# Kernel optimization log

Measured on AMD Instinct MI355X. Metric: run time of the kernel, lower is better.

Reference implementation:

```python
import jax, jax.numpy as jnp
import numpy as np

B, T, I, H, C, S = 512, 128, 512, 512, 97, 26  # batch, enc_len, input, hidden, classes, num_steps


def setup_inputs() -> dict:
    key = jax.random.key(0)
    ks = jax.random.split(key, 12)
    s = 0.05
    d = {}
    d["batch_H"] = jax.random.normal(ks[0], (B, T, I), dtype=jnp.float32)
    d["text"] = jax.random.randint(ks[1], (B, S), 0, C)
    # attention cell params
    d["W_feat"] = jax.random.normal(ks[2], (H, I), dtype=jnp.float32) * s   # feature_projection (no bias)
    d["W_hid"] = jax.random.normal(ks[3], (H, H), dtype=jnp.float32) * s    # hidden_projection
    d["b_hid"] = jnp.zeros((H,), dtype=jnp.float32)
    d["w_score"] = jax.random.normal(ks[4], (H,), dtype=jnp.float32) * s    # attention_score (Linear(H,1), no bias)
    # LSTMCell params, PyTorch gate order [i, f, g, o]
    d["W_ih"] = jax.random.normal(ks[5], (4 * H, I + C), dtype=jnp.float32) * s
    d["W_hh"] = jax.random.normal(ks[6], (4 * H, H), dtype=jnp.float32) * s
    d["b_ih"] = jnp.zeros((4 * H,), dtype=jnp.float32)
    d["b_hh"] = jnp.zeros((4 * H,), dtype=jnp.float32)
    # generator
    d["W_gen"] = jax.random.normal(ks[7], (C, H), dtype=jnp.float32) * s
    d["b_gen"] = jnp.zeros((C,), dtype=jnp.float32)
    return d


def reference(batch_H, text, W_feat, W_hid, b_hid, w_score, W_ih, W_hh, b_ih, b_hh, W_gen, b_gen):
    Bb, Tt, _ = batch_H.shape
    Hh = W_hid.shape[0]
    Cc = W_gen.shape[0]
    # step-invariant: project encoder features once  [B, T, H]
    feat = jnp.einsum('bti,hi->bth', batch_H, W_feat)
    onehots = jax.nn.one_hot(text, Cc, dtype=batch_H.dtype)  # [B, S, C]

    def step(carry, oh):
        h, c = carry
        hp = h @ W_hid.T + b_hid                                     # [B, H]
        e = jnp.einsum('bth,h->bt', jnp.tanh(feat + hp[:, None, :]), w_score)
        alpha = jax.nn.softmax(e, axis=1)                            # [B, T]
        ctx = jnp.einsum('bt,bti->bi', alpha, batch_H)               # [B, I]
        x = jnp.concatenate([ctx, oh], axis=1)                       # [B, I+C]
        gates = x @ W_ih.T + b_ih + h @ W_hh.T + b_hh                # [B, 4H]
        i_g, f_g, g_g, o_g = jnp.split(gates, 4, axis=1)
        c2 = jax.nn.sigmoid(f_g) * c + jax.nn.sigmoid(i_g) * jnp.tanh(g_g)
        h2 = jax.nn.sigmoid(o_g) * jnp.tanh(c2)
        return (h2, c2), h2

    init = (jnp.zeros((Bb, Hh), dtype=batch_H.dtype), jnp.zeros((Bb, Hh), dtype=batch_H.dtype))
    _, hs = jax.lax.scan(step, init, jnp.swapaxes(onehots, 0, 1))    # hs: [S, B, H]
    out_h = jnp.swapaxes(hs, 0, 1)                                   # [B, S, H]
    probs = out_h @ W_gen.T + b_gen                                  # [B, S, C]
    return probs
```

## Files before the change

### kernel.cpp

```cpp
#include <hip/hip_runtime.h>
#include <hip/hip_bf16.h>
#include <stdint.h>
#include <stddef.h>

typedef __bf16 bf16;
typedef __bf16 v8bf __attribute__((ext_vector_type(8)));
typedef float  v4f  __attribute__((ext_vector_type(4)));

#define B_ 512
#define T_ 128
#define I_ 512
#define H_ 512
#define C_ 97
#define S_ 26

__device__ __forceinline__ void async_copy16(void* lds, const void* g) {
  __builtin_amdgcn_global_load_lds((__attribute__((address_space(1))) void*)g,
                                   (__attribute__((address_space(3))) void*)lds,
                                   16, 0, 0);
}

__device__ __forceinline__ float fast_tanh(float x) {
  float e = __expf(2.0f * x);
  return fmaf(-2.0f, __builtin_amdgcn_rcpf(e + 1.0f), 1.0f);
}
__device__ __forceinline__ float fast_sigmoid(float x) {
  float t = __expf(-x);
  return __builtin_amdgcn_rcpf(1.0f + t);
}

__device__ __forceinline__ void zero_acc(v4f acc[4][4]) {
  v4f z = {0.f, 0.f, 0.f, 0.f};
#pragma unroll
  for (int i = 0; i < 4; ++i)
#pragma unroll
    for (int j = 0; j < 4; ++j) acc[i][j] = z;
}

#define WAITBAR(N)                                             \
  do {                                                         \
    asm volatile("s_waitcnt vmcnt(" #N ")" ::: "memory");      \
    __builtin_amdgcn_s_barrier();                              \
    __builtin_amdgcn_sched_barrier(0);                         \
  } while (0)

template <int KTOT>
__device__ __forceinline__ void mm_qb32(const bf16* aRow0, const bf16* aRow1,
                                        const bf16* bRow0, const bf16* bRow1,
                                        bf16* As, bf16* Bs, int tid,
                                        v4f acc[4][4]) {
  constexpr int NT = KTOT / 32;
  const int wave = tid >> 6, lane = tid & 63;
  const int wr = (wave >> 1) * 64, wc = (wave & 1) * 64;
  const int fr = lane & 15, fq = lane >> 4;
  const int s0 = tid * 8;
  const int aB = (wr + fr) * 32 + fq * 8;
  const int bB = (wc + fr) * 32 + fq * 8;
#define STG32(bi, kk)                                   \
  do {                                                  \
    const int o = (bi) * 4096 + s0;                     \
    async_copy16(As + o, aRow0 + (kk));                 \
    async_copy16(As + o + 2048, aRow1 + (kk));          \
    async_copy16(Bs + o, bRow0 + (kk));                 \
    async_copy16(Bs + o + 2048, bRow1 + (kk));          \
  } while (0)
  STG32(0, 0);
  STG32(1, 32);
  for (int t = 0; t < NT; ++t) {
    if (t + 2 < NT) {
      STG32((t + 2) & 3, (t + 2) * 32);
      WAITBAR(8);
    } else if (t + 1 < NT) {
      WAITBAR(4);
    } else {
      WAITBAR(0);
    }
    const int cb = (t & 3) * 4096;
    v8bf av[4], bv[4];
#pragma unroll
    for (int i = 0; i < 4; ++i) av[i] = *(const v8bf*)(As + cb + aB + i * 512);
#pragma unroll
    for (int j = 0; j < 4; ++j) bv[j] = *(const v8bf*)(Bs + cb + bB + j * 512);
    __builtin_amdgcn_s_setprio(1);
#pragma unroll
    for (int i = 0; i < 4; ++i) {
#pragma unroll
      for (int j = 0; j < 4; ++j) {
        acc[i][j] = __builtin_amdgcn_mfma_f32_16x16x32_bf16(av[i], bv[j], acc[i][j], 0, 0, 0);
      }
    }
    __builtin_amdgcn_s_setprio(0);
  }
#undef STG32
}

template <int KTOT>
__device__ __forceinline__ void mm_reg_f32a(const float* aR0, const float* aR1,
                                            const bf16* bRow0, const bf16* bRow1,
                                            bf16* As, bf16* Bs, int tid,
                                            v4f acc[4][4]) {
  const int wave = tid >> 6, lane = tid & 63;
  const int wr = (wave >> 1) * 64, wc = (wave & 1) * 64;
  const int fr = lane & 15, fq = lane >> 4;
  bf16* a_s0 = As + tid * 8;
  bf16* a_s1 = As + (tid + 256) * 8;
  bf16* b_s0 = Bs + tid * 8;
  bf16* b_s1 = Bs + (tid + 256) * 8;
  const bf16* aF[4];
  const bf16* bF[4];
#pragma unroll
  for (int i = 0; i < 4; ++i) {
    aF[i] = As + (wr + i * 16 + fr) * 32 + fq * 8;
    bF[i] = Bs + (wc + i * 16 + fr) * 32 + fq * 8;
  }
  for (int kk = 0; kk < KTOT; kk += 32) {
    v8bf va0, va1;
    const float* p0 = aR0 + kk;
    const float* p1 = aR1 + kk;
    v4f f00 = ((const v4f*)p0)[0], f01 = ((const v4f*)p0)[1];
    v4f f10 = ((const v4f*)p1)[0], f11 = ((const v4f*)p1)[1];
#pragma unroll
    for (int j = 0; j < 4; ++j) {
      va0[j] = (bf16)f00[j]; va0[j + 4] = (bf16)f01[j];
      va1[j] = (bf16)f10[j]; va1[j + 4] = (bf16)f11[j];
    }
    v8bf vb0 = *(const v8bf*)(bRow0 + kk);
    v8bf vb1 = *(const v8bf*)(bRow1 + kk);
    __syncthreads();
    *(v8bf*)a_s0 = va0;
    *(v8bf*)a_s1 = va1;
    *(v8bf*)b_s0 = vb0;
    *(v8bf*)b_s1 = vb1;
    __syncthreads();
    v8bf av[4], bv[4];
#pragma unroll
    for (int i = 0; i < 4; ++i) av[i] = *(const v8bf*)aF[i];
#pragma unroll
    for (int j = 0; j < 4; ++j) bv[j] = *(const v8bf*)bF[j];
#pragma unroll
    for (int i = 0; i < 4; ++i) {
#pragma unroll
      for (int j = 0; j < 4; ++j) {
        acc[i][j] = __builtin_amdgcn_mfma_f32_16x16x32_bf16(av[i], bv[j], acc[i][j], 0, 0, 0);
      }
    }
  }
  __syncthreads();
}

__global__ void k_prep_all(const float* __restrict__ batch_H, bf16* __restrict__ bH16, int nbh,
                           const float* __restrict__ W_feat, bf16* __restrict__ Wf16,
                           const float* __restrict__ W_hid, bf16* __restrict__ Whid16,
                           const float* __restrict__ Wih, const float* __restrict__ Whh,
                           bf16* __restrict__ Wcat,
                           const float* __restrict__ Wg, bf16* __restrict__ Wgen16,
                           float* __restrict__ OHT) {
  int b = blockIdx.x;
  const int t = threadIdx.x;
  if (b < nbh) {
    int i = (b * 256 + t) * 4;
    v4f f = *(const v4f*)(batch_H + i);
#pragma unroll
    for (int j = 0; j < 4; ++j) bH16[i + j] = (bf16)f[j];
    return;
  }
  b -= nbh;
  if (b < 256) {
    int i = (b * 256 + t) * 4;
    v4f f = *(const v4f*)(W_feat + i);
#pragma unroll
    for (int j = 0; j < 4; ++j) Wf16[i + j] = (bf16)f[j];
  } else if (b < 512) {
    int i = ((b - 256) * 256 + t) * 4;
    v4f f = *(const v4f*)(W_hid + i);
#pragma unroll
    for (int j = 0; j < 4; ++j) Whid16[i + j] = (bf16)f[j];
  } else if (b < 2560) {
    int n = b - 512;
#pragma unroll
    for (int j = 0; j < 4; ++j) {
      int k = t * 4 + j;
      float v = (k < 512) ? Wih[(size_t)n * 609 + k] : Whh[(size_t)n * 512 + (k - 512)];
      Wcat[(size_t)n * 1024 + k] = (bf16)v;
    }
  } else if (b < 2688) {
    int row = b - 2560;
#pragma unroll
    for (int j = 0; j < 2; ++j) {
      int k = t * 2 + j;
      float v = (row < C_) ? Wg[(size_t)row * 512 + k] : 0.0f;
      Wgen16[(size_t)row * 512 + k] = (bf16)v;
    }
  } else {
    int n = (b - 2688) * 256 + t;
    const float* src = Wih + (size_t)n * 609 + 512;
    for (int c = 0; c < C_; ++c) OHT[(size_t)c * 2048 + n] = src[c];
  }
}


__global__ __launch_bounds__(256, 2) void k_feat16(const bf16* __restrict__ A,
                                                   const bf16* __restrict__ Bw,
                                                   bf16* __restrict__ F) {
  __shared__ bf16 As[4 * 4096];
  __shared__ bf16 Bs[4 * 4096];
  const int tid = threadIdx.x;
  const int m0 = blockIdx.x * 128, n0 = blockIdx.y * 128;
  const int r0 = tid >> 2, k0 = (tid & 3) * 8;
  const bf16* aRow0 = A + (size_t)(m0 + r0) * 512 + k0;
  const bf16* aRow1 = A + (size_t)(m0 + r0 + 64) * 512 + k0;
  const bf16* bRow0 = Bw + (size_t)(n0 + r0) * 512 + k0;
  const bf16* bRow1 = Bw + (size_t)(n0 + r0 + 64) * 512 + k0;
  v4f acc[4][4];
  zero_acc(acc);
  mm_qb32<512>(aRow0, aRow1, bRow0, bRow1, As, Bs, tid, acc);
  const int wave = tid >> 6, lane = tid & 63;
  const int wr = (wave >> 1) * 64, wc = (wave & 1) * 64;
  const int fr = lane & 15, fq = lane >> 4;
#pragma unroll
  for (int i = 0; i < 4; ++i) {
#pragma unroll
    for (int j = 0; j < 4; ++j) {
      int col = n0 + wc + j * 16 + fr;
#pragma unroll
      for (int r = 0; r < 4; ++r) {
        int row = m0 + wr + i * 16 + fq * 4 + r;
        F[(size_t)row * 512 + col] = (bf16)acc[i][j][r];
      }
    }
  }
}

__global__ __launch_bounds__(256, 2) void k_feat32(const float* __restrict__ A,
                                                   const bf16* __restrict__ Bw,
                                                   bf16* __restrict__ F) {
  __shared__ bf16 As[128 * 32];
  __shared__ bf16 Bs[128 * 32];
  const int tid = threadIdx.x;
  const int m0 = blockIdx.x * 128, n0 = blockIdx.y * 128;
  const int r0 = tid >> 2, k0 = (tid & 3) * 8;
  const float* aRow0 = A + (size_t)(m0 + r0) * 512 + k0;
  const float* aRow1 = A + (size_t)(m0 + r0 + 64) * 512 + k0;
  const bf16* bRow0 = Bw + (size_t)(n0 + r0) * 512 + k0;
  const bf16* bRow1 = Bw + (size_t)(n0 + r0 + 64) * 512 + k0;
  v4f acc[4][4];
  zero_acc(acc);
  mm_reg_f32a<512>(aRow0, aRow1, bRow0, bRow1, As, Bs, tid, acc);
  const int wave = tid >> 6, lane = tid & 63;
  const int wr = (wave >> 1) * 64, wc = (wave & 1) * 64;
  const int fr = lane & 15, fq = lane >> 4;
#pragma unroll
  for (int i = 0; i < 4; ++i) {
#pragma unroll
    for (int j = 0; j < 4; ++j) {
      int col = n0 + wc + j * 16 + fr;
#pragma unroll
      for (int r = 0; r < 4; ++r) {
        int row = m0 + wr + i * 16 + fq * 4 + r;
        F[(size_t)row * 512 + col] = (bf16)acc[i][j][r];
      }
    }
  }
}

__global__ __launch_bounds__(256) void k_hp(const bf16* __restrict__ xb_cur,
                                            const bf16* __restrict__ Whid16,
                                            const float* __restrict__ b_hid,
                                            float* __restrict__ P) {
  __shared__ bf16 As[4 * 2048];
  __shared__ bf16 Bs[4 * 4096];
  const int tid = threadIdx.x, wave = tid >> 6, lane = tid & 63;
  const int flat = blockIdx.x;
  const int m0 = (flat >> 3) * 32;
  const int n0 = (flat & 7) * 64;
  const int fr = lane & 15, fq = lane >> 4;
  const int ra = tid >> 3, sa = (tid & 7) ^ (ra & 7);
  const bf16* aSrc = xb_cur + (size_t)(m0 + ra) * 1024 + 512 + sa * 8;
  const int rb0 = tid >> 3, rb1 = (tid >> 3) + 32;
  const bf16* bSrc0 = Whid16 + (size_t)(n0 + rb0) * 512 + (((tid & 7) ^ (rb0 & 7)) * 8);
  const bf16* bSrc1 = Whid16 + (size_t)(n0 + rb1) * 512 + (((tid & 7) ^ (rb1 & 7)) * 8);
  const int s0 = tid * 8;
  v4f acc[2];
  v4f z = {0.f, 0.f, 0.f, 0.f};
  acc[0] = z; acc[1] = z;
#define STGH(bi, kk)                                    \
  do {                                                  \
    async_copy16(As + (bi) * 2048 + s0, aSrc + (kk));   \
    async_copy16(Bs + (bi) * 4096 + s0, bSrc0 + (kk));  \
    async_copy16(Bs + (bi) * 4096 + 2048 + s0, bSrc1 + (kk)); \
  } while (0)
  STGH(0, 0);
  STGH(1, 64);
  constexpr int NT = 8;
  for (int t = 0; t < NT; ++t) {
    if (t + 2 < NT) {
      STGH((t + 2) & 3, (t + 2) * 64);
      WAITBAR(6);
    } else if (t + 1 < NT) {
      WAITBAR(3);
    } else {
      WAITBAR(0);
    }
    const int cb4 = (t & 3) * 2048;
    const int cb8 = (t & 3) * 4096;
#pragma unroll
    for (int ks = 0; ks < 2; ++ks) {
      const int sw = ((ks * 4 + fq) ^ (fr & 7)) * 8;
      v8bf bv = *(const v8bf*)(Bs + cb8 + (wave * 16 + fr) * 64 + sw);
      __builtin_amdgcn_s_setprio(1);
#pragma unroll
      for (int i = 0; i < 2; ++i) {
        v8bf av = *(const v8bf*)(As + cb4 + (i * 16 + fr) * 64 + sw);
        acc[i] = __builtin_amdgcn_mfma_f32_16x16x32_bf16(av, bv, acc[i], 0, 0, 0);
      }
      __builtin_amdgcn_s_setprio(0);
    }
  }
#undef STGH
  const int col = n0 + wave * 16 + fr;
  const float bh = b_hid[col];
#pragma unroll
  for (int i = 0; i < 2; ++i) {
#pragma unroll
    for (int r = 0; r < 4; ++r) {
      int row = m0 + i * 16 + fq * 4 + r;
      P[(size_t)row * 512 + col] = acc[i][r] + bh;
    }
  }
}

template <bool CTX16>
__global__ __launch_bounds__(512, 4) void k_attn(const bf16* __restrict__ F,
                                                 const float* __restrict__ P,
                                                 const float* __restrict__ w_score,
                                                 const void* __restrict__ bHv,
                                                 bf16* __restrict__ xb_cur) {
  const int b = blockIdx.x;
  const int tid = threadIdx.x, wave = tid >> 6, lane = tid & 63;
  __shared__ float e_s[T_];
  __shared__ float red[8][I_];
  const float CF = 2.8853900817779268f;
  float pl[8], Wv[8];
  {
    const float* p = P + (size_t)b * H_ + lane * 8;
#pragma unroll
    for (int j = 0; j < 8; ++j) pl[j] = CF * p[j];
    const float* w = w_score + lane * 8;
#pragma unroll
    for (int j = 0; j < 8; ++j) Wv[j] = w[j];
  }
  float sW = 0.f;
#pragma unroll
  for (int j = 0; j < 8; ++j) sW += Wv[j];
#pragma unroll
  for (int off = 32; off; off >>= 1) sW += __shfl_xor(sW, off, 64);
  const bf16* Fb = F + (size_t)b * T_ * H_ + lane * 8;
#pragma unroll
  for (int kb = 0; kb < 2; ++kb) {
    v8bf r[8];
#pragma unroll
    for (int u = 0; u < 8; ++u)
      r[u] = *(const v8bf*)(Fb + (size_t)(wave + kb * 64 + u * 8) * H_);
    float a[8];
#pragma unroll
    for (int u = 0; u < 8; ++u) {
      float s = 0.f;
#pragma unroll
      for (int j = 0; j < 8; ++j)
        s = fmaf(Wv[j], __builtin_amdgcn_rcpf(1.0f + exp2f(fmaf(CF, (float)r[u][j], pl[j]))), s);
      a[u] = s;
    }
#pragma unroll
    for (int off = 32; off; off >>= 1) {
#pragma unroll
      for (int u = 0; u < 8; ++u) a[u] += __shfl_xor(a[u], off, 64);
    }
    if (lane == 0) {
#pragma unroll
      for (int u = 0; u < 8; ++u) e_s[wave + kb * 64 + u * 8] = sW - 2.0f * a[u];
    }
  }
  __syncthreads();
  const int i0 = lane * 8;
  float c[8];
#pragma unroll
  for (int j = 0; j < 8; ++j) c[j] = 0.f;
  if (CTX16) {
    const bf16* hb = (const bf16*)bHv + (size_t)b * T_ * I_ + i0;
    v8bf p[8];
#pragma unroll
    for (int u = 0; u < 8; ++u)
      p[u] = *(const v8bf*)(hb + (size_t)(wave + u * 8) * I_);
    float x0, x1;
    {
      float e0 = e_s[lane], e1 = e_s[lane + 64];
      float m = fmaxf(e0, e1);
#pragma unroll
      for (int off = 32; off; off >>= 1) m = fmaxf(m, __shfl_xor(m, off, 64));
      x0 = __expf(e0 - m);
      x1 = __expf(e1 - m);
      float ssum = x0 + x1;
#pragma unroll
      for (int off = 32; off; off >>= 1) ssum += __shfl_xor(ssum, off, 64);
      float inv = __builtin_amdgcn_rcpf(ssum);
      x0 *= inv;
      x1 *= inv;
    }
    float aa[8];
#pragma unroll
    for (int u = 0; u < 8; ++u) aa[u] = __shfl(x0, wave + u * 8, 64);
    v8bf p2[8];
#pragma unroll
    for (int u = 0; u < 8; ++u)
      p2[u] = *(const v8bf*)(hb + (size_t)(64 + wave + u * 8) * I_);
#pragma unroll
    for (int u = 0; u < 8; ++u) {
#pragma unroll
      for (int j = 0; j < 8; ++j) c[j] = fmaf(aa[u], (float)p[u][j], c[j]);
    }
#pragma unroll
    for (int u = 0; u < 8; ++u) aa[u] = __shfl(x1, wave + u * 8, 64);
#pragma unroll
    for (int u = 0; u < 8; ++u) {
#pragma unroll
      for (int j = 0; j < 8; ++j) c[j] = fmaf(aa[u], (float)p2[u][j], c[j]);
    }
  } else {
    float x0, x1;
    {
      float e0 = e_s[lane], e1 = e_s[lane + 64];
      float m = fmaxf(e0, e1);
#pragma unroll
      for (int off = 32; off; off >>= 1) m = fmaxf(m, __shfl_xor(m, off, 64));
      x0 = __expf(e0 - m);
      x1 = __expf(e1 - m);
      float ssum = x0 + x1;
#pragma unroll
      for (int off = 32; off; off >>= 1) ssum += __shfl_xor(ssum, off, 64);
      float inv = __builtin_amdgcn_rcpf(ssum);
      x0 *= inv;
      x1 *= inv;
    }
    const float* hf = (const float*)bHv + (size_t)b * T_ * I_ + i0;
#pragma unroll
    for (int k = 0; k < 4; ++k) {
      const int t = wave + 32 * k;
      float xa = (k < 2) ? x0 : x1;
      float aa0 = __shfl(xa, t & 63, 64);
      float aa1 = __shfl(xa, (t + 8) & 63, 64);
      float aa2 = __shfl(xa, (t + 16) & 63, 64);
      float aa3 = __shfl(xa, (t + 24) & 63, 64);
      const float* p0 = hf + (size_t)t * I_;
      const float* p1 = hf + (size_t)(t + 8) * I_;
      const float* p2 = hf + (size_t)(t + 16) * I_;
      const float* p3 = hf + (size_t)(t + 24) * I_;
      v4f q00 = ((const v4f*)p0)[0], q01 = ((const v4f*)p0)[1];
      v4f q10 = ((const v4f*)p1)[0], q11 = ((const v4f*)p1)[1];
      v4f q20 = ((const v4f*)p2)[0], q21 = ((const v4f*)p2)[1];
      v4f q30 = ((const v4f*)p3)[0], q31 = ((const v4f*)p3)[1];
#pragma unroll
      for (int j = 0; j < 4; ++j) {
        c[j]     = fmaf(aa0, q00[j], c[j]);
        c[j + 4] = fmaf(aa0, q01[j], c[j + 4]);
        c[j]     = fmaf(aa1, q10[j], c[j]);
        c[j + 4] = fmaf(aa1, q11[j], c[j + 4]);
        c[j]     = fmaf(aa2, q20[j], c[j]);
        c[j + 4] = fmaf(aa2, q21[j], c[j + 4]);
        c[j]     = fmaf(aa3, q30[j], c[j]);
        c[j + 4] = fmaf(aa3, q31[j], c[j + 4]);
      }
    }
  }
#pragma unroll
  for (int j = 0; j < 8; ++j) red[wave][i0 + j] = c[j];
  __syncthreads();
  {
    int i = tid;
    float s = red[0][i] + red[1][i] + red[2][i] + red[3][i] +
              red[4][i] + red[5][i] + red[6][i] + red[7][i];
    xb_cur[(size_t)b * 1024 + i] = (bf16)s;
  }
}

__global__ __launch_bounds__(256) void k_gates(const bf16* __restrict__ xb_cur,
                                               const bf16* __restrict__ Wcat,
                                               const float* __restrict__ OHT,
                                               const float* __restrict__ b_ih,
                                               const float* __restrict__ b_hh,
                                               const int* __restrict__ text,
                                               float* __restrict__ c_state,
                                               bf16* __restrict__ out_h,
                                               bf16* __restrict__ xb_nxt, int s) {
  __shared__ union {
    struct { bf16 A[4 * 2048]; bf16 Bv[4 * 8192]; } st;
    float Cs[32 * 132];
  } sm;
  const int tid = threadIdx.x;
  const int flat = blockIdx.x;
  const int xcd = flat & 7;
  const int idx = flat >> 3;
  const int m0 = (idx >> 1) * 32;
  const int j0 = (xcd * 2 + (idx & 1)) * 32;
  const int wave = tid >> 6, lane = tid & 63;
  const int fr = lane & 15, fq = lane >> 4;
  const int s0 = tid * 8;
  const int ra = tid >> 3, sa = (tid & 7) ^ (ra & 7);
  const bf16* aSrc = xb_cur + (size_t)(m0 + ra) * 1024 + sa * 8;
  const bf16* bSrc[4];
#pragma unroll
  for (int cc = 0; cc < 4; ++cc) {
    const int rb = (tid >> 3) + cc * 32;
    const int nw = (rb >> 5) * 512 + j0 + (rb & 31);
    bSrc[cc] = Wcat + (size_t)nw * 1024 + (((tid & 7) ^ (rb & 7)) * 8);
  }
  v4f acc[2][2];
  {
    v4f z = {0.f, 0.f, 0.f, 0.f};
    acc[0][0] = z; acc[0][1] = z; acc[1][0] = z; acc[1][1] = z;
  }
#define STGG(bi, kk)                                                 \
  do {                                                               \
    async_copy16(sm.st.A + (bi) * 2048 + s0, aSrc + (kk));           \
    async_copy16(sm.st.Bv + (bi) * 8192 + s0, bSrc[0] + (kk));       \
    async_copy16(sm.st.Bv + (bi) * 8192 + 2048 + s0, bSrc[1] + (kk)); \
    async_copy16(sm.st.Bv + (bi) * 8192 + 4096 + s0, bSrc[2] + (kk)); \
    async_copy16(sm.st.Bv + (bi) * 8192 + 6144 + s0, bSrc[3] + (kk)); \
  } while (0)
  STGG(0, 0);
  STGG(1, 64);
  constexpr int NT = 16;
  for (int t = 0; t < NT; ++t) {
    if (t + 2 < NT) {
      STGG((t + 2) & 3, (t + 2) * 64);
      WAITBAR(10);
    } else if (t + 1 < NT) {
      WAITBAR(5);
    } else {
      WAITBAR(0);
    }
    const int ca = (t & 3) * 2048;
    const int cbv = (t & 3) * 8192;
#pragma unroll
    for (int ks = 0; ks < 2; ++ks) {
      const int sw = ((ks * 4 + fq) ^ (fr & 7)) * 8;
      v8bf av[2], bv[2];
#pragma unroll
      for (int i = 0; i < 2; ++i)
        av[i] = *(const v8bf*)(sm.st.A + ca + (i * 16 + fr) * 64 + sw);
#pragma unroll
      for (int jf = 0; jf < 2; ++jf)
        bv[jf] = *(const v8bf*)(sm.st.Bv + cbv + (wave * 32 + jf * 16 + fr) * 64 + sw);
      __builtin_amdgcn_s_setprio(1);
#pragma unroll
      for (int i = 0; i < 2; ++i)
#pragma unroll
        for (int jf = 0; jf < 2; ++jf)
          acc[i][jf] = __builtin_amdgcn_mfma_f32_16x16x32_bf16(av[i], bv[jf], acc[i][jf], 0, 0, 0);
      __builtin_amdgcn_s_setprio(0);
    }
  }
#undef STGG
  __syncthreads();
  int tcv[2][4];
#pragma unroll
  for (int i = 0; i < 2; ++i)
#pragma unroll
    for (int r = 0; r < 4; ++r)
      tcv[i][r] = text[(size_t)(m0 + i * 16 + fq * 4 + r) * S_ + s];
#pragma unroll
  for (int jf = 0; jf < 2; ++jf) {
    int cl = wave * 32 + jf * 16 + fr;
    int nw = (cl >> 5) * 512 + j0 + (cl & 31);
    float bias = b_ih[nw] + b_hh[nw];
    const float* oh = OHT + nw;
#pragma unroll
    for (int i = 0; i < 2; ++i) {
#pragma unroll
      for (int r = 0; r < 4; ++r) {
        int rl = i * 16 + fq * 4 + r;
        sm.Cs[rl * 132 + cl] = acc[i][jf][r] + bias + oh[(size_t)tcv[i][r] * 2048];
      }
    }
  }
  __syncthreads();
#pragma unroll
  for (int it = 0; it < 4; ++it) {
    int idx2 = tid + it * 256;
    int r = idx2 >> 5, q = idx2 & 31;
    float ig = sm.Cs[r * 132 + q];
    float fg = sm.Cs[r * 132 + 32 + q];
    float gg = sm.Cs[r * 132 + 64 + q];
    float og = sm.Cs[r * 132 + 96 + q];
    size_t cix = (size_t)(m0 + r) * 512 + j0 + q;
    float c2 = fast_sigmoid(fg) * c_state[cix] + fast_sigmoid(ig) * fast_tanh(gg);
    float h2 = fast_sigmoid(og) * fast_tanh(c2);
    c_state[cix] = c2;
    bf16 hb = (bf16)h2;
    xb_nxt[(size_t)(m0 + r) * 1024 + 512 + j0 + q] = hb;
    out_h[((size_t)(m0 + r) * S_ + s) * 512 + j0 + q] = hb;
  }
}

__global__ __launch_bounds__(256) void k_gen(const bf16* __restrict__ out_h,
                                             const bf16* __restrict__ Wgen16,
                                             const float* __restrict__ b_gen,
                                             float* __restrict__ out) {
  __shared__ bf16 As[4 * 4096];
  __shared__ bf16 Bs[4 * 4096];
  const int tid = threadIdx.x;
  const int m0 = blockIdx.x * 128;
  const int r0 = tid >> 2, k0 = (tid & 3) * 8;
  const bf16* aRow0 = out_h + (size_t)(m0 + r0) * 512 + k0;
  const bf16* aRow1 = out_h + (size_t)(m0 + r0 + 64) * 512 + k0;
  const bf16* bRow0 = Wgen16 + (size_t)r0 * 512 + k0;
  const bf16* bRow1 = Wgen16 + (size_t)(r0 + 64) * 512 + k0;
  v4f acc[4][4];
  zero_acc(acc);
  mm_qb32<512>(aRow0, aRow1, bRow0, bRow1, As, Bs, tid, acc);
  const int wave = tid >> 6, lane = tid & 63;
  const int wr = (wave >> 1) * 64, wc = (wave & 1) * 64;
  const int fr = lane & 15, fq = lane >> 4;
#pragma unroll
  for (int i = 0; i < 4; ++i) {
#pragma unroll
    for (int j = 0; j < 4; ++j) {
      int col = wc + j * 16 + fr;
      if (col < C_) {
        float bg = b_gen[col];
#pragma unroll
        for (int r = 0; r < 4; ++r) {
          int row = m0 + wr + i * 16 + fq * 4 + r;
          out[(size_t)row * C_ + col] = acc[i][j][r] + bg;
        }
      }
    }
  }
}

extern "C" void kernel_launch(void* const* d_in, const int* in_sizes, int n_in,
                              void* d_out, int out_size, void* d_ws, size_t ws_size,
                              hipStream_t stream) {
  (void)in_sizes; (void)n_in; (void)out_size;
  const float* batch_H = (const float*)d_in[0];
  const int*   text    = (const int*)d_in[1];
  const float* W_feat  = (const float*)d_in[2];
  const float* W_hid   = (const float*)d_in[3];
  const float* b_hid   = (const float*)d_in[4];
  const float* w_score = (const float*)d_in[5];
  const float* W_ih    = (const float*)d_in[6];
  const float* W_hh    = (const float*)d_in[7];
  const float* b_ih    = (const float*)d_in[8];
  const float* b_hh    = (const float*)d_in[9];
  const float* W_gen   = (const float*)d_in[10];
  const float* b_gen   = (const float*)d_in[11];
  float* out = (float*)d_out;

  char* ws = (char*)d_ws;
  bf16*  F       = (bf16*)(ws);
  bf16*  out_h   = (bf16*)(ws + 67108864);
  float* P       = (float*)(ws + 80740352);
  bf16*  xb0     = (bf16*)(ws + 81788928);
  bf16*  xb1     = (bf16*)(ws + 82837504);
  float* c_state = (float*)(ws + 83886080);
  bf16*  Wcat    = (bf16*)(ws + 84934656);
  bf16*  Wf16    = (bf16*)(ws + 89128960);
  bf16*  Whid16  = (bf16*)(ws + 89653248);
  bf16*  Wgen16  = (bf16*)(ws + 90177536);
  float* OHT     = (float*)(ws + 90308608);
  bf16*  bH16    = (bf16*)(ws + 91357184);
  const bool useBH16 = (ws_size >= (size_t)158466048);

  bf16* xb[2] = {xb0, xb1};

  hipMemsetAsync(xb0, 0, (size_t)512 * 1024 * 2, stream);
  hipMemsetAsync(c_state, 0, (size_t)512 * 512 * 4, stream);

  const int nbh = useBH16 ? 32768 : 0;
  k_prep_all<<<dim3(nbh + 2696), 256, 0, stream>>>(
      batch_H, bH16, nbh, W_feat, Wf16, W_hid, Whid16,
      W_ih, W_hh, Wcat, W_gen, Wgen16, OHT);

  if (useBH16) {
    k_feat16<<<dim3(512, 4), 256, 0, stream>>>(bH16, Wf16, F);
  } else {
    k_feat32<<<dim3(512, 4), 256, 0, stream>>>(batch_H, Wf16, F);
  }

  for (int s = 0; s < S_; ++s) {
    bf16* cur = xb[s & 1];
    bf16* nxt = xb[(s + 1) & 1];
    k_hp<<<dim3(128), 256, 0, stream>>>(cur, Whid16, b_hid, P);
    if (useBH16) {
      k_attn<true><<<dim3(512), 512, 0, stream>>>(F, P, w_score, bH16, cur);
    } else {
      k_attn<false><<<dim3(512), 512, 0, stream>>>(F, P, w_score, batch_H, cur);
    }
    k_gates<<<dim3(256), 256, 0, stream>>>(cur, Wcat, OHT, b_ih, b_hh, text,
                                           c_state, out_h, nxt, s);
  }
  k_gen<<<dim3(104, 1), 256, 0, stream>>>(out_h, Wgen16, b_gen, out);
}
```

Before: 1.441 ms.

## Split attention into parallel score kernel and context kernel; vectorize prep conversions

The fused per-batch attention kernel becomes two kernels. The first spreads the tanh-score computation over 2048 blocks (four per batch row) and writes scores to a scratch buffer, reusing the next-step xb buffer. The second does softmax and the context reduction. The prep kernel is reordered so the slow OHT transpose blocks launch first, and its bf16 conversions are vectorized to 8- and 4-element packed stores. This adds a kernel launch and a global round-trip of the scores each step, in exchange for more parallelism on the transcendental-heavy score phase.

Measured after the change: 1.478 ms. 2.5% more time.

```diff
diff --git a/kernel.cpp b/kernel.cpp
--- a/kernel.cpp
+++ b/kernel.cpp
@@ -35,6 +35,19 @@
   for (int i = 0; i < 4; ++i)
 #pragma unroll
     for (int j = 0; j < 4; ++j) acc[i][j] = z;
+}
+
+__device__ __forceinline__ void store_bf16x8(bf16* dst, v4f a, v4f b) {
+  union { bf16 h[8]; uint4 u; } pk;
+#pragma unroll
+  for (int j = 0; j < 4; ++j) { pk.h[j] = (bf16)a[j]; pk.h[4 + j] = (bf16)b[j]; }
+  *(uint4*)dst = pk.u;
+}
+__device__ __forceinline__ void store_bf16x4(bf16* dst, float a0, float a1,
+                                             float a2, float a3) {
+  union { bf16 h[4]; uint2 u; } pk;
+  pk.h[0] = (bf16)a0; pk.h[1] = (bf16)a1; pk.h[2] = (bf16)a2; pk.h[3] = (bf16)a3;
+  *(uint2*)dst = pk.u;
 }
 
 #define WAITBAR(N)                                             \
@@ -148,7 +161,7 @@
   __syncthreads();
 }
 
-__global__ void k_prep_all(const float* __restrict__ batch_H, bf16* __restrict__ bH16, int nbh,
+__global__ void k_prep_all(const float* __restrict__ batch_H, bf16* __restrict__ bH16, int nbhb,
                            const float* __restrict__ W_feat, bf16* __restrict__ Wf16,
                            const float* __restrict__ W_hid, bf16* __restrict__ Whid16,
                            const float* __restrict__ Wih, const float* __restrict__ Whh,
@@ -157,44 +170,61 @@
                            float* __restrict__ OHT) {
   int b = blockIdx.x;
   const int t = threadIdx.x;
-  if (b < nbh) {
-    int i = (b * 256 + t) * 4;
-    v4f f = *(const v4f*)(batch_H + i);
-#pragma unroll
-    for (int j = 0; j < 4; ++j) bH16[i + j] = (bf16)f[j];
+  if (b < 8) {
+    int n = b * 256 + t;
+    const float* src = Wih + (size_t)n * 609 + 512;
+#pragma unroll 8
+    for (int c = 0; c < C_; ++c) OHT[(size_t)c * 2048 + n] = src[c];
     return;
   }
-  b -= nbh;
-  if (b < 256) {
-    int i = (b * 256 + t) * 4;
-    v4f f = *(const v4f*)(W_feat + i);
-#pragma unroll
-    for (int j = 0; j < 4; ++j) Wf16[i + j] = (bf16)f[j];
-  } else if (b < 512) {
-    int i = ((b - 256) * 256 + t) * 4;
-    v4f f = *(const v4f*)(W_hid + i);
-#pragma unroll
-    for (int j = 0; j < 4; ++j) Whid16[i + j] = (bf16)f[j];
-  } else if (b < 2560) {
-    int n = b - 512;
-#pragma unroll
-    for (int j = 0; j < 4; ++j) {
-      int k = t * 4 + j;
-      float v = (k < 512) ? Wih[(size_t)n * 609 + k] : Whh[(size_t)n * 512 + (k - 512)];
-      Wcat[(size_t)n * 1024 + k] = (bf16)v;
-    }
-  } else if (b < 2688) {
-    int row = b - 2560;
-#pragma unroll
-    for (int j = 0; j < 2; ++j) {
-      int k = t * 2 + j;
-      float v = (row < C_) ? Wg[(size_t)row * 512 + k] : 0.0f;
-      Wgen16[(size_t)row * 512 + k] = (bf16)v;
-    }
-  } else {
-    int n = (b - 2688) * 256 + t;
-    const float* src = Wih + (size_t)n * 609 + 512;
-    for (int c = 0; c < C_; ++c) OHT[(size_t)c * 2048 + n] = src[c];
+  b -= 8;
+  if (b < 128) {
+    int row = b;
+    int k = t * 2;
+    float v0 = (row < C_) ? Wg[(size_t)row * 512 + k] : 0.0f;
+    float v1 = (row < C_) ? Wg[(size_t)row * 512 + k + 1] : 0.0f;
+    union { bf16 h[2]; uint u; } pk;
+    pk.h[0] = (bf16)v0; pk.h[1] = (bf16)v1;
+    *(uint*)(Wgen16 + (size_t)row * 512 + k) = pk.u;
+    return;
+  }
+  b -= 128;
+  if (b < 2048) {
+    int n = b;
+    int k = t * 4;
+    float v0, v1, v2, v3;
+    if (k < 512) {
+      const float* s = Wih + (size_t)n * 609 + k;
+      v0 = s[0]; v1 = s[1]; v2 = s[2]; v3 = s[3];
+    } else {
+      const float* s = Whh + (size_t)n * 512 + (k - 512);
+      v0 = s[0]; v1 = s[1]; v2 = s[2]; v3 = s[3];
+    }
+    store_bf16x4(Wcat + (size_t)n * 1024 + k, v0, v1, v2, v3);
+    return;
+  }
+  b -= 2048;
+  if (b < 128) {
+    int i = (b * 256 + t) * 8;
+    v4f f0 = ((const v4f*)(W_feat + i))[0];
+    v4f f1 = ((const v4f*)(W_feat + i))[1];
+    store_bf16x8(Wf16 + i, f0, f1);
+    return;
+  }
+  b -= 128;
+  if (b < 128) {
+    int i = (b * 256 + t) * 8;
+    v4f f0 = ((const v4f*)(W_hid + i))[0];
+    v4f f1 = ((const v4f*)(W_hid + i))[1];
+    store_bf16x8(Whid16 + i, f0, f1);
+    return;
+  }
+  b -= 128;
+  if (b < nbhb) {
+    int i = (b * 256 + t) * 8;
+    v4f f0 = ((const v4f*)(batch_H + i))[0];
+    v4f f1 = ((const v4f*)(batch_H + i))[1];
+    store_bf16x8(bH16 + i, f0, f1);
   }
 }
 
@@ -329,12 +359,124 @@
   }
 }
 
-template <bool CTX16>
-__global__ __launch_bounds__(512, 4) void k_attn(const bf16* __restrict__ F,
-                                                 const float* __restrict__ P,
-                                                 const float* __restrict__ w_score,
-                                                 const void* __restrict__ bHv,
-                                                 bf16* __restrict__ xb_cur) {
+__global__ __launch_bounds__(256, 6) void k_attn_e(const bf16* __restrict__ F,
+                                                   const float* __restrict__ P,
+                                                   const float* __restrict__ w_score,
+                                                   float* __restrict__ e_g) {
+  const int bid = blockIdx.x;
+  const int b = bid >> 2, c = bid & 3;
+  const int tid = threadIdx.x, wave = tid >> 6, lane = tid & 63;
+  const float CF = 2.8853900817779268f;
+  float pl[8], Wv[8];
+  {
+    const float* p = P + (size_t)b * H_ + lane * 8;
+#pragma unroll
+    for (int j = 0; j < 8; ++j) pl[j] = CF * p[j];
+    const float* w = w_score + lane * 8;
+#pragma unroll
+    for (int j = 0; j < 8; ++j) Wv[j] = w[j];
+  }
+  float sW = 0.f;
+#pragma unroll
+  for (int j = 0; j < 8; ++j) sW += Wv[j];
+#pragma unroll
+  for (int off = 32; off; off >>= 1) sW += __shfl_xor(sW, off, 64);
+  const bf16* Fb = F + (size_t)b * T_ * H_ + lane * 8;
+  const int t0 = c * 32 + wave * 8;
+#pragma unroll
+  for (int kb = 0; kb < 2; ++kb) {
+    v8bf r[4];
+#pragma unroll
+    for (int u = 0; u < 4; ++u)
+      r[u] = *(const v8bf*)(Fb + (size_t)(t0 + kb * 4 + u) * H_);
+    float a[4];
+#pragma unroll
+    for (int u = 0; u < 4; ++u) {
+      float s = 0.f;
+#pragma unroll
+      for (int j = 0; j < 8; ++j)
+        s = fmaf(Wv[j], __builtin_amdgcn_rcpf(1.0f + exp2f(fmaf(CF, (float)r[u][j], pl[j]))), s);
+      a[u] = s;
+    }
+#pragma unroll
+    for (int off = 32; off; off >>= 1) {
+#pragma unroll
+      for (int u = 0; u < 4; ++u) a[u] += __shfl_xor(a[u], off, 64);
+    }
+    if (lane == 0) {
+#pragma unroll
+      for (int u = 0; u < 4; ++u)
+        e_g[(size_t)b * T_ + t0 + kb * 4 + u] = sW - 2.0f * a[u];
+    }
+  }
+}
+
+__global__ __launch_bounds__(512, 4) void k_attn_ctx(const float* __restrict__ e_g,
+                                                     const bf16* __restrict__ bH,
+                                                     bf16* __restrict__ xb_cur) {
+  const int b = blockIdx.x;
+  const int tid = threadIdx.x, wave = tid >> 6, lane = tid & 63;
+  __shared__ float red[8][I_];
+  const int i0 = lane * 8;
+  const bf16* hb = bH + (size_t)b * T_ * I_ + i0;
+  v8bf p[8];
+#pragma unroll
+  for (int u = 0; u < 8; ++u)
+    p[u] = *(const v8bf*)(hb + (size_t)(wave + u * 8) * I_);
+  float x0, x1;
+  {
+    float e0 = e_g[(size_t)b * T_ + lane];
+    float e1 = e_g[(size_t)b * T_ + 64 + lane];
+    float m = fmaxf(e0, e1);
+#pragma unroll
+    for (int off = 32; off; off >>= 1) m = fmaxf(m, __shfl_xor(m, off, 64));
+    x0 = __expf(e0 - m);
+    x1 = __expf(e1 - m);
+    float ssum = x0 + x1;
+#pragma unroll
+    for (int off = 32; off; off >>= 1) ssum += __shfl_xor(ssum, off, 64);
+    float inv = __builtin_amdgcn_rcpf(ssum);
+    x0 *= inv;
+    x1 *= inv;
+  }
+  float c[8];
+#pragma unroll
+  for (int j = 0; j < 8; ++j) c[j] = 0.f;
+  float aa[8];
+#pragma unroll
+  for (int u = 0; u < 8; ++u) aa[u] = __shfl(x0, wave + u * 8, 64);
+  v8bf p2[8];
+#pragma unroll
+  for (int u = 0; u < 8; ++u)
+    p2[u] = *(const v8bf*)(hb + (size_t)(64 + wave + u * 8) * I_);
+#pragma unroll
+  for (int u = 0; u < 8; ++u) {
+#pragma unroll
+    for (int j = 0; j < 8; ++j) c[j] = fmaf(aa[u], (float)p[u][j], c[j]);
+  }
+#pragma unroll
+  for (int u = 0; u < 8; ++u) aa[u] = __shfl(x1, wave + u * 8, 64);
+#pragma unroll
+  for (int u = 0; u < 8; ++u) {
+#pragma unroll
+    for (int j = 0; j < 8; ++j) c[j] = fmaf(aa[u], (float)p2[u][j], c[j]);
+  }
+#pragma unroll
+  for (int j = 0; j < 8; ++j) red[wave][i0 + j] = c[j];
+  __syncthreads();
+  {
+    int i = tid;
+    float s = red[0][i] + red[1][i] + red[2][i] + red[3][i] +
+              red[4][i] + red[5][i] + red[6][i] + red[7][i];
+    xb_cur[(size_t)b * 1024 + i] = (bf16)s;
+  }
+}
+
+__global__ __launch_bounds__(512, 4) void k_attn_f32(const bf16* __restrict__ F,
+                                                     const float* __restrict__ P,
+                                                     const float* __restrict__ w_score,
+                                                     const float* __restrict__ bHv,
+                                                     bf16* __restrict__ xb_cur) {
   const int b = blockIdx.x;
   const int tid = threadIdx.x, wave = tid >> 6, lane = tid & 63;
   __shared__ float e_s[T_];
@@ -381,94 +523,52 @@
     }
   }
   __syncthreads();
+  float x0, x1;
+  {
+    float e0 = e_s[lane], e1 = e_s[lane + 64];
+    float m = fmaxf(e0, e1);
+#pragma unroll
+    for (int off = 32; off; off >>= 1) m = fmaxf(m, __shfl_xor(m, off, 64));
+    x0 = __expf(e0 - m);
+    x1 = __expf(e1 - m);
+    float ssum = x0 + x1;
+#pragma unroll
+    for (int off = 32; off; off >>= 1) ssum += __shfl_xor(ssum, off, 64);
+    float inv = __builtin_amdgcn_rcpf(ssum);
+    x0 *= inv;
+    x1 *= inv;
+  }
   const int i0 = lane * 8;
   float c[8];
 #pragma unroll
   for (int j = 0; j < 8; ++j) c[j] = 0.f;
-  if (CTX16) {
-    const bf16* hb = (const bf16*)bHv + (size_t)b * T_ * I_ + i0;
-    v8bf p[8];
-#pragma unroll
-    for (int u = 0; u < 8; ++u)
-      p[u] = *(const v8bf*)(hb + (size_t)(wave + u * 8) * I_);
-    float x0, x1;
-    {
-      float e0 = e_s[lane], e1 = e_s[lane + 64];
-      float m = fmaxf(e0, e1);
-#pragma unroll
-      for (int off = 32; off; off >>= 1) m = fmaxf(m, __shfl_xor(m, off, 64));
-      x0 = __expf(e0 - m);
-      x1 = __expf(e1 - m);
-      float ssum = x0 + x1;
-#pragma unroll
-      for (int off = 32; off; off >>= 1) ssum += __shfl_xor(ssum, off, 64);
-      float inv = __builtin_amdgcn_rcpf(ssum);
-      x0 *= inv;
-      x1 *= inv;
-    }
-    float aa[8];
-#pragma unroll
-    for (int u = 0; u < 8; ++u) aa[u] = __shfl(x0, wave + u * 8, 64);
-    v8bf p2[8];
-#pragma unroll
-    for (int u = 0; u < 8; ++u)
-      p2[u] = *(const v8bf*)(hb + (size_t)(64 + wave + u * 8) * I_);
-#pragma unroll
-    for (int u = 0; u < 8; ++u) {
-#pragma unroll
-      for (int j = 0; j < 8; ++j) c[j] = fmaf(aa[u], (float)p[u][j], c[j]);
-    }
-#pragma unroll
-    for (int u = 0; u < 8; ++u) aa[u] = __shfl(x1, wave + u * 8, 64);
-#pragma unroll
-    for (int u = 0; u < 8; ++u) {
-#pragma unroll
-      for (int j = 0; j < 8; ++j) c[j] = fmaf(aa[u], (float)p2[u][j], c[j]);
-    }
-  } else {
-    float x0, x1;
-    {
-      float e0 = e_s[lane], e1 = e_s[lane + 64];
-      float m = fmaxf(e0, e1);
-#pragma unroll
-      for (int off = 32; off; off >>= 1) m = fmaxf(m, __shfl_xor(m, off, 64));
-      x0 = __expf(e0 - m);
-      x1 = __expf(e1 - m);
-      float ssum = x0 + x1;
-#pragma unroll
-      for (int off = 32; off; off >>= 1) ssum += __shfl_xor(ssum, off, 64);
-      float inv = __builtin_amdgcn_rcpf(ssum);
-      x0 *= inv;
-      x1 *= inv;
-    }
-    const float* hf = (const float*)bHv + (size_t)b * T_ * I_ + i0;
-#pragma unroll
-    for (int k = 0; k < 4; ++k) {
-      const int t = wave + 32 * k;
-      float xa = (k < 2) ? x0 : x1;
-      float aa0 = __shfl(xa, t & 63, 64);
-      float aa1 = __shfl(xa, (t + 8) & 63, 64);
-      float aa2 = __shfl(xa, (t + 16) & 63, 64);
-      float aa3 = __shfl(xa, (t + 24) & 63, 64);
-      const float* p0 = hf + (size_t)t * I_;
-      const float* p1 = hf + (size_t)(t + 8) * I_;
-      const float* p2 = hf + (size_t)(t + 16) * I_;
-      const float* p3 = hf + (size_t)(t + 24) * I_;
-      v4f q00 = ((const v4f*)p0)[0], q01 = ((const v4f*)p0)[1];
-      v4f q10 = ((const v4f*)p1)[0], q11 = ((const v4f*)p1)[1];
-      v4f q20 = ((const v4f*)p2)[0], q21 = ((const v4f*)p2)[1];
-      v4f q30 = ((const v4f*)p3)[0], q31 = ((const v4f*)p3)[1];
-#pragma unroll
-      for (int j = 0; j < 4; ++j) {
-        c[j]     = fmaf(aa0, q00[j], c[j]);
-        c[j + 4] = fmaf(aa0, q01[j], c[j + 4]);
-        c[j]     = fmaf(aa1, q10[j], c[j]);
-        c[j + 4] = fmaf(aa1, q11[j], c[j + 4]);
-        c[j]     = fmaf(aa2, q20[j], c[j]);
-        c[j + 4] = fmaf(aa2, q21[j], c[j + 4]);
-        c[j]     = fmaf(aa3, q30[j], c[j]);
-        c[j + 4] = fmaf(aa3, q31[j], c[j + 4]);
-      }
+  const float* hf = bHv + (size_t)b * T_ * I_ + i0;
+#pragma unroll
+  for (int k = 0; k < 4; ++k) {
+    const int t = wave + 32 * k;
+    float xa = (k < 2) ? x0 : x1;
+    float aa0 = __shfl(xa, t & 63, 64);
+    float aa1 = __shfl(xa, (t + 8) & 63, 64);
+    float aa2 = __shfl(xa, (t + 16) & 63, 64);
+    float aa3 = __shfl(xa, (t + 24) & 63, 64);
+    const float* p0 = hf + (size_t)t * I_;
+    const float* p1 = hf + (size_t)(t + 8) * I_;
+    const float* p2 = hf + (size_t)(t + 16) * I_;
+    const float* p3 = hf + (size_t)(t + 24) * I_;
+    v4f q00 = ((const v4f*)p0)[0], q01 = ((const v4f*)p0)[1];
+    v4f q10 = ((const v4f*)p1)[0], q11 = ((const v4f*)p1)[1];
+    v4f q20 = ((const v4f*)p2)[0], q21 = ((const v4f*)p2)[1];
+    v4f q30 = ((const v4f*)p3)[0], q31 = ((const v4f*)p3)[1];
+#pragma unroll
+    for (int j = 0; j < 4; ++j) {
+      c[j]     = fmaf(aa0, q00[j], c[j]);
+      c[j + 4] = fmaf(aa0, q01[j], c[j + 4]);
+      c[j]     = fmaf(aa1, q10[j], c[j]);
+      c[j + 4] = fmaf(aa1, q11[j], c[j + 4]);
+      c[j]     = fmaf(aa2, q20[j], c[j]);
+      c[j + 4] = fmaf(aa2, q21[j], c[j + 4]);
+      c[j]     = fmaf(aa3, q30[j], c[j]);
+      c[j + 4] = fmaf(aa3, q31[j], c[j + 4]);
     }
   }
 #pragma unroll
@@ -675,9 +775,9 @@
   hipMemsetAsync(xb0, 0, (size_t)512 * 1024 * 2, stream);
   hipMemsetAsync(c_state, 0, (size_t)512 * 512 * 4, stream);
 
-  const int nbh = useBH16 ? 32768 : 0;
-  k_prep_all<<<dim3(nbh + 2696), 256, 0, stream>>>(
-      batch_H, bH16, nbh, W_feat, Wf16, W_hid, Whid16,
+  const int nbhb = useBH16 ? 16384 : 0;
+  k_prep_all<<<dim3(2440 + nbhb), 256, 0, stream>>>(
+      batch_H, bH16, nbhb, W_feat, Wf16, W_hid, Whid16,
       W_ih, W_hh, Wcat, W_gen, Wgen16, OHT);
 
   if (useBH16) {
@@ -691,9 +791,11 @@
     bf16* nxt = xb[(s + 1) & 1];
     k_hp<<<dim3(128), 256, 0, stream>>>(cur, Whid16, b_hid, P);
     if (useBH16) {
-      k_attn<true><<<dim3(512), 512, 0, stream>>>(F, P, w_score, bH16, cur);
+      float* e_g = (float*)nxt;
+      k_attn_e<<<dim3(2048), 256, 0, stream>>>(F, P, w_score, e_g);
+      k_attn_ctx<<<dim3(512), 512, 0, stream>>>(e_g, bH16, cur);
     } else {
-      k_attn<false><<<dim3(512), 512, 0, stream>>>(F, P, w_score, batch_H, cur);
+      k_attn_f32<<<dim3(512), 512, 0, stream>>>(F, P, w_score, batch_H, cur);
     }
     k_gates<<<dim3(256), 256, 0, stream>>>(cur, Wcat, OHT, b_ih, b_hh, text,
                                            c_state, out_h, nxt, s);
```
